# Performance work log

Measured on AMD Instinct MI355X. Metric: run time of the kernel, lower is better.

The kernel has to match this reference:

```python
import jax, jax.numpy as jnp
import numpy as np
from jax import lax

DETER, STOCH, UNITS, ADIM, EMBED = 4096, 512, 1024, 2, 4096
B, T = 16, 64
ACTION_CLIP = 1.0


def setup_inputs() -> dict:
    key = jax.random.key(0)
    ks = jax.random.split(key, 16)
    s = 0.02
    f32 = jnp.float32
    return {
        "embed": jax.random.normal(ks[0], (B, T, EMBED), f32),
        "action": jax.random.normal(ks[1], (B, T, ADIM), f32),
        "is_first": jax.random.randint(ks[2], (B, T), 0, 2).astype(jnp.int32),
        # learned initial deter state
        "initial_deter": jnp.zeros((DETER,), f32),
        # obs_out: Linear(deter+4096 -> units)
        "w_obs": (jax.random.normal(ks[3], (UNITS, DETER + EMBED), f32) * s),
        "b_obs": jnp.zeros((UNITS,), f32),
        # img_in: Linear(stoch+action_dim -> units)
        "w_imgin": (jax.random.normal(ks[4], (UNITS, STOCH + ADIM), f32) * s),
        "b_imgin": jnp.zeros((UNITS,), f32),
        # img_out: Linear(deter -> units)
        "w_imgout": (jax.random.normal(ks[5], (UNITS, DETER), f32) * s),
        "b_imgout": jnp.zeros((UNITS,), f32),
        # GRUCell params (torch layout: [3*hidden, in] with r,z,n gate order)
        "w_ih": (jax.random.normal(ks[6], (3 * DETER, UNITS), f32) * s),
        "w_hh": (jax.random.normal(ks[7], (3 * DETER, DETER), f32) * s),
        "b_ih": jnp.zeros((3 * DETER,), f32),
        "b_hh": jnp.zeros((3 * DETER,), f32),
        # reparameterization noise for prior/post rsample at each step
        "eps_prior": jax.random.normal(ks[8], (T, B, STOCH), f32),
        "eps_post": jax.random.normal(ks[9], (T, B, STOCH), f32),
    }


def _stats(x):
    mean, std = jnp.split(x, 2, axis=-1)
    std = 2.0 * jax.nn.sigmoid(std / 2.0) + 0.1
    return mean, jnp.maximum(std, 1e-4)  # clamp from get_dist


def _gru(x, h, w_ih, w_hh, b_ih, b_hh):
    gi = x @ w_ih.T + b_ih  # [B, 3*deter]
    gh = h @ w_hh.T + b_hh
    ir, iz, inn = jnp.split(gi, 3, axis=-1)
    hr, hz, hn = jnp.split(gh, 3, axis=-1)
    r = jax.nn.sigmoid(ir + hr)
    z = jax.nn.sigmoid(iz + hz)
    n = jnp.tanh(inn + r * hn)
    return (1.0 - z) * n + z * h


def reference(embed, action, is_first, initial_deter, w_obs, b_obs,
              w_imgin, b_imgin, w_imgout, b_imgout,
              w_ih, w_hh, b_ih, b_hh, eps_prior, eps_post):
    bsz = action.shape[0]
    # initial_state (learned)
    deter0 = jnp.broadcast_to(jnp.tanh(initial_deter)[None, :], (bsz, DETER))
    m0, _ = _stats(deter0 @ w_imgout.T + b_imgout)
    stoch0 = m0  # dist.mean

    def step(carry, xs):
        deter, stoch = carry
        a, emb, first, ep, eo = xs  # [B,A], [B,E], [B], [B,S], [B,S]
        # action clip
        a = a * (ACTION_CLIP / jnp.maximum(jnp.abs(a), ACTION_CLIP))
        mask = (1.0 - first.astype(jnp.float32))[:, None]
        deter_m = deter * mask
        stoch_m = stoch * mask
        a = a * mask
        # img_step
        x = jnp.concatenate([stoch_m, a], axis=-1) @ w_imgin.T + b_imgin
        d_new = _gru(x, deter_m, w_ih, w_hh, b_ih, b_hh)
        pmean, pstd = _stats(d_new @ w_imgout.T + b_imgout)
        pstoch = pmean + pstd * ep
        # obs part
        z = jnp.concatenate([d_new, emb], axis=-1) @ w_obs.T + b_obs
        omean, ostd = _stats(z)
        ostoch = omean + ostd * eo
        out = jnp.concatenate(
            [ostoch, omean, ostd, d_new, pstoch, pmean, pstd, d_new], axis=-1)
        return (d_new, ostoch), out

    xs = (jnp.swapaxes(action, 0, 1), jnp.swapaxes(embed, 0, 1),
          jnp.swapaxes(is_first, 0, 1), eps_prior, eps_post)
    _, outs = lax.scan(step, (deter0, stoch0), xs)  # [T, B, F]
    return jnp.swapaxes(outs, 0, 1)  # [B, T, F]
```

## Files before the change

### kernel.cpp

```cpp
#include <hip/hip_runtime.h>
#include <math.h>

#define B_ 16
#define T_ 64
#define DETER_ 4096
#define STOCH_ 512
#define UNITS_ 1024
#define EMBED_ 4096
#define FOUT_ 11264

enum { JOB_IMGIN=0, JOB_GATES=1, JOB_PRIOR=2, JOB_OBS=3, JOB_PRIOR_INIT=4 };

struct SP {
  const float* embed; const float* action; const int* is_first;
  const float* wpad_imgin; const float* b_imgin;
  const float* w_ih; const float* w_hh; const float* b_ih; const float* b_hh;
  const float* w_imgout; const float* b_imgout;
  const float* w_obs; const float* b_obs;
  const float* eps_prior; const float* eps_post;
  const float* deter_m_in;
  float*       deter_m_out;
  float*       dnew;
  float* stoch_m; float* x_img; float* out;
  int t;
};

__device__ __forceinline__ float4 ld4(const float* p){ return *reinterpret_cast<const float4*>(p); }
__device__ __forceinline__ float sigm(float x){ return 1.f/(1.f+expf(-x)); }
__device__ __forceinline__ float dot4(float4 w, float4 x, float a){
  return fmaf(w.x,x.x, fmaf(w.y,x.y, fmaf(w.z,x.z, fmaf(w.w,x.w, a))));
}

__device__ __forceinline__ void g2l16(const float* g, float* l) {
  __builtin_amdgcn_global_load_lds(
      (const __attribute__((address_space(1))) unsigned int*)g,
      (__attribute__((address_space(3))) unsigned int*)l, 16, 0, 0);
}

template<int JOB>
__device__ __forceinline__ void stage_async(const SP& p, float* Xs, int c,
                                            int wave, int lane, int tid, int t) {
  __syncthreads();
  constexpr int SEGS = (JOB==JOB_IMGIN) ? 2 : 4;
  #pragma unroll
  for (int q=0;q<4;++q) {
    const int b = wave*4+q;
    const float* src;
    if constexpr (JOB==JOB_GATES)
      src = (c==0) ? (p.x_img + b*UNITS_) : (p.deter_m_in + b*DETER_ + (c-1)*1024);
    else if constexpr (JOB==JOB_PRIOR || JOB==JOB_PRIOR_INIT)
      src = p.dnew + b*DETER_ + c*1024;
    else if constexpr (JOB==JOB_OBS)
      src = (c<4) ? (p.dnew + b*DETER_ + c*1024)
                  : (p.embed + ((size_t)(b*T_+t))*EMBED_ + (c-4)*1024);
    else
      src = p.stoch_m + b*STOCH_;
    float* dst = Xs + b*1024;
    #pragma unroll
    for (int seg=0;seg<SEGS;++seg)
      g2l16(src + seg*256 + lane*4, dst + seg*256);
  }
  if constexpr (JOB==JOB_IMGIN) {
    const int kc = tid*4;
    if (kc >= 512) {
      #pragma unroll
      for (int b=0;b<16;++b) {
        float4 v = make_float4(0.f,0.f,0.f,0.f);
        if (kc == 512) {
          float mb = p.is_first[b*T_+t] ? 0.f : 1.f;
          const float* ap = p.action + (b*T_+t)*2;
          float a0 = ap[0], a1 = ap[1];
          v.x = (a0 / fmaxf(fabsf(a0),1.f))*mb;
          v.y = (a1 / fmaxf(fabsf(a1),1.f))*mb;
        }
        *reinterpret_cast<float4*>(Xs + b*1024 + kc) = v;
      }
    }
  }
  __syncthreads();
}

__device__ __forceinline__ void gates_body(const SP& p, int bid, float* Xs) {
  const int tid = threadIdx.x;
  const int wave = tid>>6, lane = tid&63;
  const int half = lane>>5, sl = lane&31;
  const int t = p.t;
  const int j = bid*4 + wave;

  float ar[8], az[8], anx[8], anh[8];
  #pragma unroll
  for (int b=0;b<8;++b){ ar[b]=0.f; az[b]=0.f; anx[b]=0.f; anh[b]=0.f; }

#define GATES_INNER(WR,WZ,WN,AN)                                           \
  _Pragma("unroll")                                                        \
  for (int it=0; it<8; ++it) {                                             \
    const int k0 = it*128 + sl*4;                                          \
    float4 w_r = ld4((WR)+k0), w_z = ld4((WZ)+k0), w_n = ld4((WN)+k0);     \
    _Pragma("unroll")                                                      \
    for (int b=0;b<8;++b) {                                                \
      float4 xv = ld4(Xs + (half*8+b)*1024 + k0);                          \
      ar[b] = dot4(w_r, xv, ar[b]);                                        \
      az[b] = dot4(w_z, xv, az[b]);                                        \
      AN[b] = dot4(w_n, xv, AN[b]);                                        \
    }                                                                      \
  }

  stage_async<JOB_GATES>(p, Xs, 0, wave, lane, tid, t);
  {
    const float* wr = p.w_ih + (size_t)j*1024;
    const float* wz = p.w_ih + (size_t)(DETER_+j)*1024;
    const float* wn = p.w_ih + (size_t)(2*DETER_+j)*1024;
    GATES_INNER(wr, wz, wn, anx)
  }
  for (int c=1;c<5;++c) {
    stage_async<JOB_GATES>(p, Xs, c, wave, lane, tid, t);
    const size_t base = (size_t)(c-1)*1024;
    const float* wr = p.w_hh + (size_t)j*4096 + base;
    const float* wz = p.w_hh + (size_t)(DETER_+j)*4096 + base;
    const float* wn = p.w_hh + (size_t)(2*DETER_+j)*4096 + base;
    GATES_INNER(wr, wz, wn, anh)
  }
#undef GATES_INNER

  #pragma unroll
  for (int off=1; off<32; off<<=1) {
    #pragma unroll
    for (int b=0;b<8;++b) {
      ar[b]  += __shfl_xor(ar[b],  off);
      az[b]  += __shfl_xor(az[b],  off);
      anx[b] += __shfl_xor(anx[b], off);
      anh[b] += __shfl_xor(anh[b], off);
    }
  }
  __syncthreads();
  if (sl==0) {
    #pragma unroll
    for (int b=0;b<8;++b) {
      Xs[(wave*4+0)*16 + half*8 + b] = ar[b];
      Xs[(wave*4+1)*16 + half*8 + b] = az[b];
      Xs[(wave*4+2)*16 + half*8 + b] = anx[b];
      Xs[(wave*4+3)*16 + half*8 + b] = anh[b];
    }
  }
  __syncthreads();

  if (tid < 64) {
    int u = tid&3, b = tid>>2;
    int jj = bid*4 + u;
    const float* res = Xs;
    float rs = res[(u*4+0)*16+b] + p.b_ih[jj]          + p.b_hh[jj];
    float zs = res[(u*4+1)*16+b] + p.b_ih[DETER_+jj]   + p.b_hh[DETER_+jj];
    float ni = res[(u*4+2)*16+b] + p.b_ih[2*DETER_+jj];
    float nh = res[(u*4+3)*16+b] + p.b_hh[2*DETER_+jj];
    float rg = sigm(rs), zg = sigm(zs);
    float ng = tanhf(ni + rg*nh);
    float hp = p.deter_m_in[b*DETER_+jj];
    float d  = (1.f-zg)*ng + zg*hp;
    p.dnew[b*DETER_+jj] = d;
    int tn = t+1;
    float mb2 = (tn<T_) ? (p.is_first[b*T_+tn] ? 0.f : 1.f) : 0.f;
    p.deter_m_out[b*DETER_+jj] = d*mb2;
    size_t ob = ((size_t)(b*T_+t))*FOUT_;
    p.out[ob+1536+jj] = d;
    p.out[ob+7168+jj] = d;
  }
}

template<int JOB>
__device__ __forceinline__ void mv_body(const SP& p, int bid, float* Xs) {
  constexpr int KTOT = (JOB==JOB_IMGIN)?1024:((JOB==JOB_OBS)?8192:4096);
  constexpr int CHUNKS = KTOT/1024;
  const int tid = threadIdx.x;
  const int wave = tid>>6, lane = tid&63;
  const int half = lane>>5, sl = lane&31;
  const int t = p.t;

  float acc[2][8];
  #pragma unroll
  for (int r=0;r<2;++r)
    #pragma unroll
    for (int b=0;b<8;++b) acc[r][b]=0.f;

  int rowIdx[2];
  #pragma unroll
  for (int r=0;r<2;++r) {
    int rl = wave*2 + r;
    if constexpr (JOB==JOB_IMGIN || JOB==JOB_PRIOR_INIT) rowIdx[r] = bid*8 + rl;
    else rowIdx[r] = (rl<4) ? (bid*4+rl) : (512 + bid*4 + (rl-4));
  }

  for (int c=0;c<CHUNKS;++c) {
    stage_async<JOB>(p, Xs, c, wave, lane, tid, t);
    const float* w0; const float* w1;
    if constexpr (JOB==JOB_IMGIN) {
      w0 = p.wpad_imgin + (size_t)rowIdx[0]*1024;
      w1 = p.wpad_imgin + (size_t)rowIdx[1]*1024;
    } else if constexpr (JOB==JOB_PRIOR || JOB==JOB_PRIOR_INIT) {
      w0 = p.w_imgout + (size_t)rowIdx[0]*4096 + (size_t)c*1024;
      w1 = p.w_imgout + (size_t)rowIdx[1]*4096 + (size_t)c*1024;
    } else {
      w0 = p.w_obs + (size_t)rowIdx[0]*8192 + (size_t)c*1024;
      w1 = p.w_obs + (size_t)rowIdx[1]*8192 + (size_t)c*1024;
    }
    #pragma unroll
    for (int it=0; it<8; ++it) {
      const int k0 = it*128 + sl*4;
      float4 wa = ld4(w0 + k0), wb2 = ld4(w1 + k0);
      #pragma unroll
      for (int b=0;b<8;++b) {
        float4 xv = ld4(Xs + (half*8+b)*1024 + k0);
        acc[0][b] = dot4(wa,  xv, acc[0][b]);
        acc[1][b] = dot4(wb2, xv, acc[1][b]);
      }
    }
  }

  #pragma unroll
  for (int off=1; off<32; off<<=1)
    #pragma unroll
    for (int r=0;r<2;++r)
      #pragma unroll
      for (int b=0;b<8;++b)
        acc[r][b] += __shfl_xor(acc[r][b], off);
  __syncthreads();
  if (sl==0) {
    #pragma unroll
    for (int r=0;r<2;++r)
      #pragma unroll
      for (int b=0;b<8;++b)
        Xs[(wave*2+r)*16 + half*8 + b] = acc[r][b];
  }
  __syncthreads();
  const float* res = Xs;

  if constexpr (JOB==JOB_PRIOR) {
    if (tid < 64) {
      int rl = tid&3, b = tid>>2;
      int j = bid*4 + rl;
      float mean = res[rl*16+b]     + p.b_imgout[j];
      float sr   = res[(rl+4)*16+b] + p.b_imgout[512+j];
      float sd = 2.f*sigm(sr*0.5f) + 0.1f; sd = fmaxf(sd, 1e-4f);
      float ep = p.eps_prior[((size_t)t*B_+b)*STOCH_ + j];
      size_t ob = ((size_t)(b*T_+t))*FOUT_;
      p.out[ob+5632+j] = fmaf(sd, ep, mean);
      p.out[ob+6144+j] = mean;
      p.out[ob+6656+j] = sd;
    }
  } else if constexpr (JOB==JOB_OBS) {
    if (tid < 64) {
      int rl = tid&3, b = tid>>2;
      int j = bid*4 + rl;
      float mean = res[rl*16+b]     + p.b_obs[j];
      float sr   = res[(rl+4)*16+b] + p.b_obs[512+j];
      float sd = 2.f*sigm(sr*0.5f) + 0.1f; sd = fmaxf(sd, 1e-4f);
      float eo = p.eps_post[((size_t)t*B_+b)*STOCH_ + j];
      float ost = fmaf(sd, eo, mean);
      size_t ob = ((size_t)(b*T_+t))*FOUT_;
      p.out[ob+0+j]    = ost;
      p.out[ob+512+j]  = mean;
      p.out[ob+1024+j] = sd;
      int tn = t+1;
      float mb2 = (tn<T_) ? (p.is_first[b*T_+tn] ? 0.f : 1.f) : 0.f;
      p.stoch_m[b*STOCH_+j] = ost*mb2;
    }
  } else if constexpr (JOB==JOB_IMGIN) {
    if (tid < 128) {
      int rl = tid&7, b = tid>>3;
      int row = bid*8 + rl;
      p.x_img[b*UNITS_+row] = res[rl*16+b] + p.b_imgin[row];
    }
  } else {
    if (tid < 128) {
      int rl = tid&7, b = tid>>3;
      int row = bid*8 + rl;
      float mean = res[rl*16+b] + p.b_imgout[row];
      float mb = p.is_first[b*T_+0] ? 0.f : 1.f;
      p.stoch_m[b*STOCH_+row] = mean*mb;
    }
  }
}

__global__ __launch_bounds__(256,2) void gates_kernel(SP p) {
  __shared__ float Xs[16*1024];
  gates_body(p, blockIdx.x, Xs);
}

template<int JOB>
__global__ __launch_bounds__(256,2) void mv_single(SP p) {
  __shared__ float Xs[16*1024];
  mv_body<JOB>(p, blockIdx.x, Xs);
}

__global__ __launch_bounds__(256,2) void post_kernel(SP p) {
  __shared__ float Xs[16*1024];
  if (blockIdx.x < 128) mv_body<JOB_PRIOR>(p, blockIdx.x, Xs);
  else                  mv_body<JOB_OBS>(p, blockIdx.x - 128, Xs);
}

__global__ void pad_imgin_kernel(const float* w, float* wpad) {
  int row = blockIdx.x;
  for (int k=threadIdx.x; k<1024; k+=256)
    wpad[row*1024+k] = (k<514) ? w[row*514+k] : 0.f;
}

__global__ void init_deter_kernel(const float* ini, float* det, float* detm,
                                  const int* is_first) {
  int k = blockIdx.x*256 + threadIdx.x;
  float v = tanhf(ini[k]);
  #pragma unroll
  for (int b=0;b<16;++b) {
    det[b*DETER_+k] = v;
    float mb = is_first[b*T_+0] ? 0.f : 1.f;
    detm[b*DETER_+k] = v*mb;
  }
}

extern "C" void kernel_launch(void* const* d_in, const int* in_sizes, int n_in,
                              void* d_out, int out_size, void* d_ws, size_t ws_size,
                              hipStream_t stream) {
  (void)in_sizes; (void)n_in; (void)out_size; (void)ws_size;
  SP p;
  p.embed     = (const float*)d_in[0];
  p.action    = (const float*)d_in[1];
  p.is_first  = (const int*)  d_in[2];
  const float* initial_deter = (const float*)d_in[3];
  p.w_obs     = (const float*)d_in[4];
  p.b_obs     = (const float*)d_in[5];
  const float* w_imgin       = (const float*)d_in[6];
  p.b_imgin   = (const float*)d_in[7];
  p.w_imgout  = (const float*)d_in[8];
  p.b_imgout  = (const float*)d_in[9];
  p.w_ih      = (const float*)d_in[10];
  p.w_hh      = (const float*)d_in[11];
  p.b_ih      = (const float*)d_in[12];
  p.b_hh      = (const float*)d_in[13];
  p.eps_prior = (const float*)d_in[14];
  p.eps_post  = (const float*)d_in[15];
  p.out = (float*)d_out;

  float* ws      = (float*)d_ws;
  float* wpad    = ws;
  float* dnew    = wpad    + 1024*1024;
  float* deterM0 = dnew    + 16*DETER_;
  float* deterM1 = deterM0 + 16*DETER_;
  float* stochm  = deterM1 + 16*DETER_;
  float* ximg    = stochm  + 16*STOCH_;
  p.wpad_imgin = wpad;
  p.stoch_m = stochm;
  p.x_img = ximg;

  pad_imgin_kernel<<<1024,256,0,stream>>>(w_imgin, wpad);
  init_deter_kernel<<<DETER_/256,256,0,stream>>>(initial_deter, dnew, deterM0, p.is_first);

  p.t = 0; p.dnew = dnew; p.deter_m_in = deterM0; p.deter_m_out = deterM1;
  mv_single<JOB_PRIOR_INIT><<<64,256,0,stream>>>(p);

  for (int t=0; t<T_; ++t) {
    p.t = t;
    p.deter_m_in  = (t&1) ? deterM1 : deterM0;
    p.deter_m_out = (t&1) ? deterM0 : deterM1;
    p.dnew        = dnew;
    mv_single<JOB_IMGIN><<<128,256,0,stream>>>(p);
    gates_kernel<<<1024,256,0,stream>>>(p);
    post_kernel<<<256,256,0,stream>>>(p);
  }
}
```

Measured before the change: 10.97 ms.

## Double-buffer async LDS staging in gates and post matvec kernels

Replaces the synchronous stage-then-compute loops in the GRU gates kernel and the prior/obs matvec kernel with double-buffered 512-wide chunks. The next chunk is loaded into LDS via global_load_lds while the current chunk is computed, using manual vmcnt waits and s_barrier. The gates kernel also grows to 512 threads covering 8 hidden units per block, which halves the block count. The aim is to hide global-to-LDS latency behind the FMA work, at the cost of more barriers per step and hand-tuned waitcnt values that are fragile.

New measurement: 11.35 ms. 3.5% more time.

```diff
diff --git a/kernel.cpp b/kernel.cpp
--- a/kernel.cpp
+++ b/kernel.cpp
@@ -37,90 +37,77 @@
       (__attribute__((address_space(3))) unsigned int*)l, 16, 0, 0);
 }
 
-template<int JOB>
-__device__ __forceinline__ void stage_async(const SP& p, float* Xs, int c,
-                                            int wave, int lane, int tid, int t) {
-  __syncthreads();
-  constexpr int SEGS = (JOB==JOB_IMGIN) ? 2 : 4;
-  #pragma unroll
-  for (int q=0;q<4;++q) {
-    const int b = wave*4+q;
-    const float* src;
-    if constexpr (JOB==JOB_GATES)
-      src = (c==0) ? (p.x_img + b*UNITS_) : (p.deter_m_in + b*DETER_ + (c-1)*1024);
-    else if constexpr (JOB==JOB_PRIOR || JOB==JOB_PRIOR_INIT)
-      src = p.dnew + b*DETER_ + c*1024;
-    else if constexpr (JOB==JOB_OBS)
-      src = (c<4) ? (p.dnew + b*DETER_ + c*1024)
-                  : (p.embed + ((size_t)(b*T_+t))*EMBED_ + (c-4)*1024);
-    else
-      src = p.stoch_m + b*STOCH_;
-    float* dst = Xs + b*1024;
-    #pragma unroll
-    for (int seg=0;seg<SEGS;++seg)
-      g2l16(src + seg*256 + lane*4, dst + seg*256);
-  }
-  if constexpr (JOB==JOB_IMGIN) {
-    const int kc = tid*4;
-    if (kc >= 512) {
-      #pragma unroll
-      for (int b=0;b<16;++b) {
-        float4 v = make_float4(0.f,0.f,0.f,0.f);
-        if (kc == 512) {
-          float mb = p.is_first[b*T_+t] ? 0.f : 1.f;
-          const float* ap = p.action + (b*T_+t)*2;
-          float a0 = ap[0], a1 = ap[1];
-          v.x = (a0 / fmaxf(fabsf(a0),1.f))*mb;
-          v.y = (a1 / fmaxf(fabsf(a1),1.f))*mb;
-        }
-        *reinterpret_cast<float4*>(Xs + b*1024 + kc) = v;
-      }
-    }
-  }
-  __syncthreads();
-}
-
-__device__ __forceinline__ void gates_body(const SP& p, int bid, float* Xs) {
+__global__ __launch_bounds__(512,4) void gates_pipe(SP p) {
+  __shared__ float Xs[16384];
+  const int bid = blockIdx.x;
   const int tid = threadIdx.x;
   const int wave = tid>>6, lane = tid&63;
   const int half = lane>>5, sl = lane&31;
   const int t = p.t;
-  const int j = bid*4 + wave;
+  const int j = bid*8 + wave;
+  float* buf0 = Xs; float* buf1 = Xs + 8192;
 
   float ar[8], az[8], anx[8], anh[8];
   #pragma unroll
   for (int b=0;b<8;++b){ ar[b]=0.f; az[b]=0.f; anx[b]=0.f; anh[b]=0.f; }
 
-#define GATES_INNER(WR,WZ,WN,AN)                                           \
-  _Pragma("unroll")                                                        \
-  for (int it=0; it<8; ++it) {                                             \
-    const int k0 = it*128 + sl*4;                                          \
-    float4 w_r = ld4((WR)+k0), w_z = ld4((WZ)+k0), w_n = ld4((WN)+k0);     \
-    _Pragma("unroll")                                                      \
-    for (int b=0;b<8;++b) {                                                \
-      float4 xv = ld4(Xs + (half*8+b)*1024 + k0);                          \
-      ar[b] = dot4(w_r, xv, ar[b]);                                        \
-      az[b] = dot4(w_z, xv, az[b]);                                        \
-      AN[b] = dot4(w_n, xv, AN[b]);                                        \
-    }                                                                      \
-  }
-
-  stage_async<JOB_GATES>(p, Xs, 0, wave, lane, tid, t);
-  {
-    const float* wr = p.w_ih + (size_t)j*1024;
-    const float* wz = p.w_ih + (size_t)(DETER_+j)*1024;
-    const float* wn = p.w_ih + (size_t)(2*DETER_+j)*1024;
-    GATES_INNER(wr, wz, wn, anx)
-  }
-  for (int c=1;c<5;++c) {
-    stage_async<JOB_GATES>(p, Xs, c, wave, lane, tid, t);
-    const size_t base = (size_t)(c-1)*1024;
-    const float* wr = p.w_hh + (size_t)j*4096 + base;
-    const float* wz = p.w_hh + (size_t)(DETER_+j)*4096 + base;
-    const float* wn = p.w_hh + (size_t)(2*DETER_+j)*4096 + base;
-    GATES_INNER(wr, wz, wn, anh)
-  }
-#undef GATES_INNER
+  auto stage = [&](float* dst, int c) {
+    #pragma unroll
+    for (int q=0;q<2;++q) {
+      const int b = wave*2+q;
+      const float* src = (c<2) ? (p.x_img + b*UNITS_ + c*512)
+                               : (p.deter_m_in + b*DETER_ + (c-2)*512);
+      g2l16(src + lane*4,       dst + b*512);
+      g2l16(src + 256 + lane*4, dst + b*512 + 256);
+    }
+  };
+
+#define GINNER(AN)                                                      \
+  _Pragma("unroll")                                                     \
+  for (int it=0; it<4; ++it) {                                          \
+    const int k0 = it*128 + sl*4;                                       \
+    float4 w_r = ld4(wr+k0), w_z = ld4(wz+k0), w_n = ld4(wn+k0);        \
+    _Pragma("unroll")                                                   \
+    for (int b=0;b<8;++b) {                                             \
+      float4 xv = ld4(cur + (half*8+b)*512 + k0);                       \
+      ar[b] = dot4(w_r, xv, ar[b]);                                     \
+      az[b] = dot4(w_z, xv, az[b]);                                     \
+      AN[b] = dot4(w_n, xv, AN[b]);                                     \
+    }                                                                   \
+  }
+
+  stage(buf0, 0);
+  for (int c=0;c<10;++c) {
+    float* cur = (c&1)? buf1 : buf0;
+    float* nxt = (c&1)? buf0 : buf1;
+    __builtin_amdgcn_s_barrier();
+    __builtin_amdgcn_sched_barrier(0);
+    if (c < 9) {
+      stage(nxt, c+1);
+      __builtin_amdgcn_sched_barrier(0);
+      asm volatile("s_waitcnt vmcnt(4)" ::: "memory");
+    } else {
+      asm volatile("s_waitcnt vmcnt(0)" ::: "memory");
+    }
+    __builtin_amdgcn_sched_barrier(0);
+    __builtin_amdgcn_s_barrier();
+
+    const float *wr, *wz, *wn;
+    if (c < 2) {
+      const size_t o = (size_t)c*512;
+      wr = p.w_ih + (size_t)j*1024 + o;
+      wz = p.w_ih + (size_t)(4096+j)*1024 + o;
+      wn = p.w_ih + (size_t)(8192+j)*1024 + o;
+      GINNER(anx)
+    } else {
+      const size_t o = (size_t)(c-2)*512;
+      wr = p.w_hh + (size_t)j*4096 + o;
+      wz = p.w_hh + (size_t)(4096+j)*4096 + o;
+      wn = p.w_hh + (size_t)(8192+j)*4096 + o;
+      GINNER(anh)
+    }
+  }
+#undef GINNER
 
   #pragma unroll
   for (int off=1; off<32; off<<=1) {
@@ -132,21 +119,20 @@
       anh[b] += __shfl_xor(anh[b], off);
     }
   }
-  __syncthreads();
   if (sl==0) {
     #pragma unroll
     for (int b=0;b<8;++b) {
-      Xs[(wave*4+0)*16 + half*8 + b] = ar[b];
-      Xs[(wave*4+1)*16 + half*8 + b] = az[b];
-      Xs[(wave*4+2)*16 + half*8 + b] = anx[b];
-      Xs[(wave*4+3)*16 + half*8 + b] = anh[b];
-    }
-  }
-  __syncthreads();
-
-  if (tid < 64) {
-    int u = tid&3, b = tid>>2;
-    int jj = bid*4 + u;
+      buf0[(wave*4+0)*16 + half*8 + b] = ar[b];
+      buf0[(wave*4+1)*16 + half*8 + b] = az[b];
+      buf0[(wave*4+2)*16 + half*8 + b] = anx[b];
+      buf0[(wave*4+3)*16 + half*8 + b] = anh[b];
+    }
+  }
+  __syncthreads();
+
+  if (tid < 128) {
+    int u = tid&7, b = tid>>3;
+    int jj = bid*8 + u;
     const float* res = Xs;
     float rs = res[(u*4+0)*16+b] + p.b_ih[jj]          + p.b_hh[jj];
     float zs = res[(u*4+1)*16+b] + p.b_ih[DETER_+jj]   + p.b_hh[DETER_+jj];
@@ -167,8 +153,174 @@
 }
 
 template<int JOB>
+__device__ __forceinline__ void pipe_mv(const SP& p, int bid, float* Xs) {
+  constexpr int NC = (JOB==JOB_OBS)?16:8;
+  const int tid = threadIdx.x;
+  const int wave = tid>>6, lane = tid&63;
+  const int half = lane>>5, sl = lane&31;
+  const int t = p.t;
+  float* buf0 = Xs; float* buf1 = Xs + 8192;
+
+  float acc[2][8];
+  #pragma unroll
+  for (int r=0;r<2;++r)
+    #pragma unroll
+    for (int b=0;b<8;++b) acc[r][b]=0.f;
+
+  int row0, row1;
+  {
+    int rl0 = wave*2, rl1 = wave*2+1;
+    row0 = (rl0<4)? (bid*4+rl0) : (512 + bid*4 + (rl0-4));
+    row1 = (rl1<4)? (bid*4+rl1) : (512 + bid*4 + (rl1-4));
+  }
+
+  auto stage = [&](float* dst, int c) {
+    #pragma unroll
+    for (int q=0;q<4;++q) {
+      const int b = wave*4+q;
+      const float* src;
+      if constexpr (JOB==JOB_PRIOR) src = p.dnew + b*DETER_ + c*512;
+      else src = (c<8) ? (p.dnew + b*DETER_ + c*512)
+                       : (p.embed + ((size_t)(b*T_+t))*EMBED_ + (c-8)*512);
+      g2l16(src + lane*4,       dst + b*512);
+      g2l16(src + 256 + lane*4, dst + b*512 + 256);
+    }
+  };
+
+  stage(buf0, 0);
+  for (int c=0;c<NC;++c) {
+    float* cur = (c&1)? buf1 : buf0;
+    float* nxt = (c&1)? buf0 : buf1;
+    __builtin_amdgcn_s_barrier();
+    __builtin_amdgcn_sched_barrier(0);
+    if (c+1 < NC) {
+      stage(nxt, c+1);
+      __builtin_amdgcn_sched_barrier(0);
+      asm volatile("s_waitcnt vmcnt(8)" ::: "memory");
+    } else {
+      asm volatile("s_waitcnt vmcnt(0)" ::: "memory");
+    }
+    __builtin_amdgcn_sched_barrier(0);
+    __builtin_amdgcn_s_barrier();
+
+    const float *w0, *w1;
+    if constexpr (JOB==JOB_PRIOR) {
+      w0 = p.w_imgout + (size_t)row0*4096 + (size_t)c*512;
+      w1 = p.w_imgout + (size_t)row1*4096 + (size_t)c*512;
+    } else {
+      w0 = p.w_obs + (size_t)row0*8192 + (size_t)c*512;
+      w1 = p.w_obs + (size_t)row1*8192 + (size_t)c*512;
+    }
+    #pragma unroll
+    for (int it=0; it<4; ++it) {
+      const int k0 = it*128 + sl*4;
+      float4 wa = ld4(w0+k0), wb2 = ld4(w1+k0);
+      #pragma unroll
+      for (int b=0;b<8;++b) {
+        float4 xv = ld4(cur + (half*8+b)*512 + k0);
+        acc[0][b] = dot4(wa,  xv, acc[0][b]);
+        acc[1][b] = dot4(wb2, xv, acc[1][b]);
+      }
+    }
+  }
+
+  #pragma unroll
+  for (int off=1; off<32; off<<=1)
+    #pragma unroll
+    for (int r=0;r<2;++r)
+      #pragma unroll
+      for (int b=0;b<8;++b)
+        acc[r][b] += __shfl_xor(acc[r][b], off);
+  if (sl==0) {
+    #pragma unroll
+    for (int r=0;r<2;++r)
+      #pragma unroll
+      for (int b=0;b<8;++b)
+        buf0[(wave*2+r)*16 + half*8 + b] = acc[r][b];
+  }
+  __syncthreads();
+  const float* res = Xs;
+
+  if constexpr (JOB==JOB_PRIOR) {
+    if (tid < 64) {
+      int rl = tid&3, b = tid>>2;
+      int jj = bid*4 + rl;
+      float mean = res[rl*16+b]     + p.b_imgout[jj];
+      float sr   = res[(rl+4)*16+b] + p.b_imgout[512+jj];
+      float sd = 2.f*sigm(sr*0.5f) + 0.1f; sd = fmaxf(sd, 1e-4f);
+      float ep = p.eps_prior[((size_t)t*B_+b)*STOCH_ + jj];
+      size_t ob = ((size_t)(b*T_+t))*FOUT_;
+      p.out[ob+5632+jj] = fmaf(sd, ep, mean);
+      p.out[ob+6144+jj] = mean;
+      p.out[ob+6656+jj] = sd;
+    }
+  } else {
+    if (tid < 64) {
+      int rl = tid&3, b = tid>>2;
+      int jj = bid*4 + rl;
+      float mean = res[rl*16+b]     + p.b_obs[jj];
+      float sr   = res[(rl+4)*16+b] + p.b_obs[512+jj];
+      float sd = 2.f*sigm(sr*0.5f) + 0.1f; sd = fmaxf(sd, 1e-4f);
+      float eo = p.eps_post[((size_t)t*B_+b)*STOCH_ + jj];
+      float ost = fmaf(sd, eo, mean);
+      size_t ob = ((size_t)(b*T_+t))*FOUT_;
+      p.out[ob+0+jj]    = ost;
+      p.out[ob+512+jj]  = mean;
+      p.out[ob+1024+jj] = sd;
+      int tn = t+1;
+      float mb2 = (tn<T_) ? (p.is_first[b*T_+tn] ? 0.f : 1.f) : 0.f;
+      p.stoch_m[b*STOCH_+jj] = ost*mb2;
+    }
+  }
+}
+
+__global__ __launch_bounds__(256,2) void post_pipe(SP p) {
+  __shared__ float Xs[16384];
+  if (blockIdx.x < 128) pipe_mv<JOB_PRIOR>(p, blockIdx.x, Xs);
+  else                  pipe_mv<JOB_OBS>(p, blockIdx.x - 128, Xs);
+}
+
+template<int JOB>
+__device__ __forceinline__ void stage_async(const SP& p, float* Xs, int c,
+                                            int wave, int lane, int tid, int t) {
+  __syncthreads();
+  constexpr int SEGS = (JOB==JOB_IMGIN) ? 2 : 4;
+  #pragma unroll
+  for (int q=0;q<4;++q) {
+    const int b = wave*4+q;
+    const float* src;
+    if constexpr (JOB==JOB_PRIOR_INIT)
+      src = p.dnew + b*DETER_ + c*1024;
+    else
+      src = p.stoch_m + b*STOCH_;
+    float* dst = Xs + b*1024;
+    #pragma unroll
+    for (int seg=0;seg<SEGS;++seg)
+      g2l16(src + seg*256 + lane*4, dst + seg*256);
+  }
+  if constexpr (JOB==JOB_IMGIN) {
+    const int kc = tid*4;
+    if (kc >= 512) {
+      #pragma unroll
+      for (int b=0;b<16;++b) {
+        float4 v = make_float4(0.f,0.f,0.f,0.f);
+        if (kc == 512) {
+          float mb = p.is_first[b*T_+t] ? 0.f : 1.f;
+          const float* ap = p.action + (b*T_+t)*2;
+          float a0 = ap[0], a1 = ap[1];
+          v.x = (a0 / fmaxf(fabsf(a0),1.f))*mb;
+          v.y = (a1 / fmaxf(fabsf(a1),1.f))*mb;
+        }
+        *reinterpret_cast<float4*>(Xs + b*1024 + kc) = v;
+      }
+    }
+  }
+  __syncthreads();
+}
+
+template<int JOB>
 __device__ __forceinline__ void mv_body(const SP& p, int bid, float* Xs) {
-  constexpr int KTOT = (JOB==JOB_IMGIN)?1024:((JOB==JOB_OBS)?8192:4096);
+  constexpr int KTOT = (JOB==JOB_IMGIN)?1024:4096;
   constexpr int CHUNKS = KTOT/1024;
   const int tid = threadIdx.x;
   const int wave = tid>>6, lane = tid&63;
@@ -183,11 +335,7 @@
 
   int rowIdx[2];
   #pragma unroll
-  for (int r=0;r<2;++r) {
-    int rl = wave*2 + r;
-    if constexpr (JOB==JOB_IMGIN || JOB==JOB_PRIOR_INIT) rowIdx[r] = bid*8 + rl;
-    else rowIdx[r] = (rl<4) ? (bid*4+rl) : (512 + bid*4 + (rl-4));
-  }
+  for (int r=0;r<2;++r) rowIdx[r] = bid*8 + wave*2 + r;
 
   for (int c=0;c<CHUNKS;++c) {
     stage_async<JOB>(p, Xs, c, wave, lane, tid, t);
@@ -195,12 +343,9 @@
     if constexpr (JOB==JOB_IMGIN) {
       w0 = p.wpad_imgin + (size_t)rowIdx[0]*1024;
       w1 = p.wpad_imgin + (size_t)rowIdx[1]*1024;
-    } else if constexpr (JOB==JOB_PRIOR || JOB==JOB_PRIOR_INIT) {
+    } else {
       w0 = p.w_imgout + (size_t)rowIdx[0]*4096 + (size_t)c*1024;
       w1 = p.w_imgout + (size_t)rowIdx[1]*4096 + (size_t)c*1024;
-    } else {
-      w0 = p.w_obs + (size_t)rowIdx[0]*8192 + (size_t)c*1024;
-      w1 = p.w_obs + (size_t)rowIdx[1]*8192 + (size_t)c*1024;
     }
     #pragma unroll
     for (int it=0; it<8; ++it) {
@@ -233,37 +378,7 @@
   __syncthreads();
   const float* res = Xs;
 
-  if constexpr (JOB==JOB_PRIOR) {
-    if (tid < 64) {
-      int rl = tid&3, b = tid>>2;
-      int j = bid*4 + rl;
-      float mean = res[rl*16+b]     + p.b_imgout[j];
-      float sr   = res[(rl+4)*16+b] + p.b_imgout[512+j];
-      float sd = 2.f*sigm(sr*0.5f) + 0.1f; sd = fmaxf(sd, 1e-4f);
-      float ep = p.eps_prior[((size_t)t*B_+b)*STOCH_ + j];
-      size_t ob = ((size_t)(b*T_+t))*FOUT_;
-      p.out[ob+5632+j] = fmaf(sd, ep, mean);
-      p.out[ob+6144+j] = mean;
-      p.out[ob+6656+j] = sd;
-    }
-  } else if constexpr (JOB==JOB_OBS) {
-    if (tid < 64) {
-      int rl = tid&3, b = tid>>2;
-      int j = bid*4 + rl;
-      float mean = res[rl*16+b]     + p.b_obs[j];
-      float sr   = res[(rl+4)*16+b] + p.b_obs[512+j];
-      float sd = 2.f*sigm(sr*0.5f) + 0.1f; sd = fmaxf(sd, 1e-4f);
-      float eo = p.eps_post[((size_t)t*B_+b)*STOCH_ + j];
-      float ost = fmaf(sd, eo, mean);
-      size_t ob = ((size_t)(b*T_+t))*FOUT_;
-      p.out[ob+0+j]    = ost;
-      p.out[ob+512+j]  = mean;
-      p.out[ob+1024+j] = sd;
-      int tn = t+1;
-      float mb2 = (tn<T_) ? (p.is_first[b*T_+tn] ? 0.f : 1.f) : 0.f;
-      p.stoch_m[b*STOCH_+j] = ost*mb2;
-    }
-  } else if constexpr (JOB==JOB_IMGIN) {
+  if constexpr (JOB==JOB_IMGIN) {
     if (tid < 128) {
       int rl = tid&7, b = tid>>3;
       int row = bid*8 + rl;
@@ -280,21 +395,10 @@
   }
 }
 
-__global__ __launch_bounds__(256,2) void gates_kernel(SP p) {
-  __shared__ float Xs[16*1024];
-  gates_body(p, blockIdx.x, Xs);
-}
-
 template<int JOB>
 __global__ __launch_bounds__(256,2) void mv_single(SP p) {
   __shared__ float Xs[16*1024];
   mv_body<JOB>(p, blockIdx.x, Xs);
-}
-
-__global__ __launch_bounds__(256,2) void post_kernel(SP p) {
-  __shared__ float Xs[16*1024];
-  if (blockIdx.x < 128) mv_body<JOB_PRIOR>(p, blockIdx.x, Xs);
-  else                  mv_body<JOB_OBS>(p, blockIdx.x - 128, Xs);
 }
 
 __global__ void pad_imgin_kernel(const float* w, float* wpad) {
@@ -361,7 +465,7 @@
     p.deter_m_out = (t&1) ? deterM0 : deterM1;
     p.dnew        = dnew;
     mv_single<JOB_IMGIN><<<128,256,0,stream>>>(p);
-    gates_kernel<<<1024,256,0,stream>>>(p);
-    post_kernel<<<256,256,0,stream>>>(p);
-  }
-}
+    gates_pipe<<<512,512,0,stream>>>(p);
+    post_pipe<<<256,256,0,stream>>>(p);
+  }
+}
```
